# Kernel tuning notes

Hardware: AMD Instinct MI355X
Metric: run time of the kernel (lower is better)

The kernel has to match this reference:

```python
import jax, jax.numpy as jnp
import numpy as np

T, H, I, E, Z, TOPK = 1024, 1024, 512, 32, 8, 4
ROUTED_SCALING = 1.0


def setup_inputs() -> dict:
    key = jax.random.key(0)
    k1, k2, k3, k4 = jax.random.split(key, 4)
    return {
        "hidden_states": jax.random.normal(k1, (T, H), jnp.float32),
        "router_w": jax.random.normal(k2, (E + Z, H), jnp.float32) * 0.02,
        "correction_bias": jnp.zeros((E + Z,), jnp.float32),
        "w_gate_up": jax.random.normal(k3, (E, 2 * I, H), jnp.float32) * 0.02,
        "w_down": jax.random.normal(k4, (E, H, I), jnp.float32) * 0.02,
        "top_k": TOPK,
    }


def reference(hidden_states, router_w, correction_bias, w_gate_up, w_down, top_k):
    # hidden_states: [T, H]; router_w: [E+Z, H]; w_gate_up: [E, 2I, H]; w_down: [E, H, I]
    t, h = hidden_states.shape
    e = w_gate_up.shape[0]
    i = w_down.shape[2]
    # --- router (float32, no bias; correction bias only affects selection) ---
    logits = jnp.einsum("th,eh->te", hidden_states.astype(jnp.float32), router_w)
    scores = jax.nn.softmax(logits, axis=-1)                     # [T, E+Z]
    _, idx = jax.lax.top_k(scores + correction_bias[None, :], top_k)  # [T, k]
    w = jnp.take_along_axis(scores, idx, axis=1) * ROUTED_SCALING     # renormalize=False
    # combine matrix [T, E+Z] (sparse top-k scattered dense)
    comb = jnp.zeros((t, scores.shape[1]), jnp.float32)
    comb = comb.at[jnp.arange(t)[:, None], idx].add(w)
    comb_routed = comb[:, :e].astype(hidden_states.dtype)        # [T, E]
    zero_w = comb[:, e:].sum(-1).astype(hidden_states.dtype)     # [T] identity zero-experts
    # --- grouped SiLU-gated expert MLPs (dense all-experts reference) ---
    gu = jnp.einsum("th,eih->eti", hidden_states, w_gate_up)     # [E, T, 2I]
    hmid = jax.nn.silu(gu[..., :i]) * gu[..., i:]                # [E, T, I]
    ye = jnp.einsum("eti,ehi->eth", hmid, w_down)                # [E, T, H]
    out = jnp.einsum("te,eth->th", comb_routed, ye)
    out = out + zero_w[:, None] * hidden_states
    return out
```

## Files before the change

### kernel.cpp

```cpp
#include <hip/hip_runtime.h>
#include <hip/hip_bf16.h>
#include <math.h>

#define TT   1024
#define HH   1024
#define II   512
#define EE   32
#define NE   40
#define TOPK 4
#define CAP  1024

typedef __attribute__((ext_vector_type(4))) short short4v;
typedef __attribute__((ext_vector_type(8))) short short8v;
typedef __attribute__((ext_vector_type(4))) float floatx4;

static __device__ __forceinline__ short f2bf(float f) {
    unsigned u = __float_as_uint(f);
    unsigned r = (u + 0x7fffu + ((u >> 16) & 1u)) >> 16;
    return (short)(r & 0xffffu);
}
static __device__ __forceinline__ float bf2f(short s) {
    return __uint_as_float(((unsigned)(unsigned short)s) << 16);
}
static __device__ __forceinline__ short4v cvt4(float4 v) {
    short4v b = { f2bf(v.x), f2bf(v.y), f2bf(v.z), f2bf(v.w) };
    return b;
}

#define WS_NEED_COMBINE 12845056ull

__global__ __launch_bounds__(64) void router_kernel(
    const float* __restrict__ x, const float* __restrict__ rw,
    const float* __restrict__ bias,
    float* __restrict__ topk_w, float* __restrict__ zero_w,
    int* __restrict__ kexp, int* __restrict__ counts, int* __restrict__ slots)
{
    __shared__ float xs[HH];
    const int t = blockIdx.x;
    const int lane = threadIdx.x;

    const float4* xp = (const float4*)(x + (size_t)t * HH);
    float4* xs4 = (float4*)xs;
    #pragma unroll
    for (int i = 0; i < HH / 4 / 64; ++i) xs4[lane + 64 * i] = xp[lane + 64 * i];
    __syncthreads();

    float mylogit = -INFINITY;
    for (int e0 = 0; e0 < NE; e0 += 4) {
        const float* r0 = rw + (size_t)e0 * HH;
        float p0 = 0.f, p1 = 0.f, p2 = 0.f, p3 = 0.f;
        #pragma unroll
        for (int i = 0; i < HH / 64; ++i) {
            int h = lane + 64 * i;
            float xv = xs[h];
            p0 += xv * r0[h];
            p1 += xv * r0[HH + h];
            p2 += xv * r0[2 * HH + h];
            p3 += xv * r0[3 * HH + h];
        }
        #pragma unroll
        for (int off = 32; off > 0; off >>= 1) {
            p0 += __shfl_xor(p0, off); p1 += __shfl_xor(p1, off);
            p2 += __shfl_xor(p2, off); p3 += __shfl_xor(p3, off);
        }
        if (lane == e0)     mylogit = p0;
        if (lane == e0 + 1) mylogit = p1;
        if (lane == e0 + 2) mylogit = p2;
        if (lane == e0 + 3) mylogit = p3;
    }

    float m = mylogit;
    #pragma unroll
    for (int off = 32; off > 0; off >>= 1) m = fmaxf(m, __shfl_xor(m, off));
    float pexp = (lane < NE) ? expf(mylogit - m) : 0.f;
    float s = pexp;
    #pragma unroll
    for (int off = 32; off > 0; off >>= 1) s += __shfl_xor(s, off);
    const float score = pexp / s;

    float val = (lane < NE) ? score + bias[lane] : -INFINITY;
    int   kidx[TOPK];
    float kw[TOPK];
    #pragma unroll
    for (int k = 0; k < TOPK; ++k) {
        float v = val; int idx = lane;
        #pragma unroll
        for (int off = 32; off > 0; off >>= 1) {
            float ov = __shfl_xor(v, off);
            int   oi = __shfl_xor(idx, off);
            if (ov > v || (ov == v && oi < idx)) { v = ov; idx = oi; }
        }
        kidx[k] = idx;
        kw[k]   = __shfl(score, idx);
        if (lane == idx) val = -INFINITY;
    }

    if (lane == 0) {
        float zw = 0.f;
        #pragma unroll
        for (int k = 0; k < TOPK; ++k) {
            int slot = t * TOPK + k;
            topk_w[slot] = kw[k];
            kexp[slot]   = kidx[k];
            if (kidx[k] < EE) {
                int pos = atomicAdd(&counts[kidx[k]], 1);
                slots[kidx[k] * CAP + pos] = slot;
            } else {
                zw += kw[k];
            }
        }
        zero_w[t] = zw;
    }
}

#define GM  128
#define GNP 32
#define GK  32
#define KP  40

__global__ __launch_bounds__(256) void gate_up_kernel(
    const float* __restrict__ x, const float* __restrict__ wgu,
    const int* __restrict__ counts, const int* __restrict__ slots,
    short* __restrict__ hmid)
{
    const int e = blockIdx.y;
    const int cnt = counts[e];
    const int m_base = blockIdx.z * GM;
    if (m_base >= cnt) return;
    const int c_base = blockIdx.x * GNP;

    __shared__ short As[2][GM * KP];
    __shared__ short Bs[2][2 * GNP * KP];
    __shared__ int   sl[GM];

    const int tid = threadIdx.x;
    if (tid < GM) {
        int m = m_base + tid;
        sl[tid] = (m < cnt) ? slots[e * CAP + m] : -1;
    }
    __syncthreads();

    const int kq = tid & 7;
    const float* wb = wgu + (size_t)e * (2 * II) * HH;

    int rowA[4]; int slA[4]; const float* pAx[4];
    #pragma unroll
    for (int it = 0; it < 4; ++it) {
        rowA[it] = (tid >> 3) + 32 * it;
        int s = sl[rowA[it]];
        slA[it] = s;
        pAx[it] = x + (size_t)((s >= 0 ? s : 0) >> 2) * HH + kq * 4;
    }
    int rowB[2]; const float* pB[2];
    #pragma unroll
    for (int it = 0; it < 2; ++it) {
        rowB[it] = (tid >> 3) + 32 * it;
        int grow = (rowB[it] < GNP) ? (c_base + rowB[it]) : (II + c_base + rowB[it] - GNP);
        pB[it] = wb + (size_t)grow * HH + kq * 4;
    }

    const int lane = tid & 63;
    const int wv_  = tid >> 6;
    const int wy   = wv_ & 1;
    const int wx   = wv_ >> 1;
    const int quad = lane >> 4;
    const int mcol = lane & 15;

    floatx4 accg[4] = {};
    floatx4 accu[4] = {};

    float4 pa[4], pb[2];
    const float4 fz = make_float4(0.f, 0.f, 0.f, 0.f);

    #pragma unroll
    for (int it = 0; it < 4; ++it) pa[it] = (slA[it] >= 0) ? *(const float4*)(pAx[it]) : fz;
    #pragma unroll
    for (int it = 0; it < 2; ++it) pb[it] = *(const float4*)(pB[it]);
    #pragma unroll
    for (int it = 0; it < 4; ++it) *(short4v*)&As[0][rowA[it] * KP + kq * 4] = cvt4(pa[it]);
    #pragma unroll
    for (int it = 0; it < 2; ++it) *(short4v*)&Bs[0][rowB[it] * KP + kq * 4] = cvt4(pb[it]);
    __syncthreads();

    int p = 0;
    for (int k0 = 0; k0 < HH; k0 += GK) {
        const int kn = k0 + GK;
        const bool more = kn < HH;
        if (more) {
            #pragma unroll
            for (int it = 0; it < 4; ++it) pa[it] = (slA[it] >= 0) ? *(const float4*)(pAx[it] + kn) : fz;
            #pragma unroll
            for (int it = 0; it < 2; ++it) pb[it] = *(const float4*)(pB[it] + kn);
        }

        short8v a[4], bg, bu;
        #pragma unroll
        for (int i = 0; i < 4; ++i)
            a[i] = *(const short8v*)&As[p][(wy * 64 + i * 16 + mcol) * KP + quad * 8];
        bg = *(const short8v*)&Bs[p][(wx * 16 + mcol) * KP + quad * 8];
        bu = *(const short8v*)&Bs[p][(GNP + wx * 16 + mcol) * KP + quad * 8];
        #pragma unroll
        for (int i = 0; i < 4; ++i) {
            accg[i] = __builtin_amdgcn_mfma_f32_16x16x32_bf16(a[i], bg, accg[i], 0, 0, 0);
            accu[i] = __builtin_amdgcn_mfma_f32_16x16x32_bf16(a[i], bu, accu[i], 0, 0, 0);
        }

        if (more) {
            #pragma unroll
            for (int it = 0; it < 4; ++it) *(short4v*)&As[1 - p][rowA[it] * KP + kq * 4] = cvt4(pa[it]);
            #pragma unroll
            for (int it = 0; it < 2; ++it) *(short4v*)&Bs[1 - p][rowB[it] * KP + kq * 4] = cvt4(pb[it]);
        }
        __syncthreads();
        p ^= 1;
    }

    #pragma unroll
    for (int i = 0; i < 4; ++i) {
        #pragma unroll
        for (int r = 0; r < 4; ++r) {
            int m = wy * 64 + i * 16 + quad * 4 + r;
            int s = sl[m];
            if (s < 0) continue;
            float g = accg[i][r], u = accu[i][r];
            float valf = g * u / (1.f + __expf(-g));
            hmid[(size_t)s * II + c_base + wx * 16 + mcol] = f2bf(valf);
        }
    }
}

#define DM 128
#define DN 64

template<int WRITE_Y>
__global__ __launch_bounds__(256) void down_kernel_t(
    const short* __restrict__ hmid, const float* __restrict__ wd,
    const int* __restrict__ counts, const int* __restrict__ slots,
    const float* __restrict__ topk_w, short* __restrict__ ydown,
    float* __restrict__ out)
{
    const int e = blockIdx.y;
    const int cnt = counts[e];
    const int m_base = blockIdx.z * DM;
    if (m_base >= cnt) return;
    const int n_base = blockIdx.x * DN;

    __shared__ short As[2][DM * KP];
    __shared__ short Bs[2][DN * KP];
    __shared__ int   sl[DM];
    __shared__ float wvs[DM];

    const int tid = threadIdx.x;
    if (tid < DM) {
        int m = m_base + tid;
        int s = (m < cnt) ? slots[e * CAP + m] : -1;
        sl[tid]  = s;
        wvs[tid] = (s >= 0) ? topk_w[s] : 0.f;
    }
    __syncthreads();

    const float* wb = wd + (size_t)e * HH * II;

    const int kc = tid & 3;
    int rowA[2]; int slA[2]; const short* pAh[2];
    #pragma unroll
    for (int it = 0; it < 2; ++it) {
        rowA[it] = (tid >> 2) + 64 * it;
        int s = sl[rowA[it]];
        slA[it] = s;
        pAh[it] = hmid + (size_t)(s >= 0 ? s : 0) * II + kc * 8;
    }
    const int kq = tid & 7;
    int rowB[2]; const float* pB[2];
    #pragma unroll
    for (int it = 0; it < 2; ++it) {
        rowB[it] = (tid >> 3) + 32 * it;
        pB[it] = wb + (size_t)(n_base + rowB[it]) * II + kq * 4;
    }

    const int lane = tid & 63;
    const int wv_  = tid >> 6;
    const int wy   = wv_ & 1;
    const int wx   = wv_ >> 1;
    const int quad = lane >> 4;
    const int mcol = lane & 15;

    floatx4 acc[4][2] = {};

    short8v pa[2]; float4 pb[2];
    const short8v sz = { 0, 0, 0, 0, 0, 0, 0, 0 };

    #pragma unroll
    for (int it = 0; it < 2; ++it) pa[it] = (slA[it] >= 0) ? *(const short8v*)(pAh[it]) : sz;
    #pragma unroll
    for (int it = 0; it < 2; ++it) pb[it] = *(const float4*)(pB[it]);
    #pragma unroll
    for (int it = 0; it < 2; ++it) *(short8v*)&As[0][rowA[it] * KP + kc * 8] = pa[it];
    #pragma unroll
    for (int it = 0; it < 2; ++it) *(short4v*)&Bs[0][rowB[it] * KP + kq * 4] = cvt4(pb[it]);
    __syncthreads();

    int p = 0;
    for (int k0 = 0; k0 < II; k0 += GK) {
        const int kn = k0 + GK;
        const bool more = kn < II;
        if (more) {
            #pragma unroll
            for (int it = 0; it < 2; ++it) pa[it] = (slA[it] >= 0) ? *(const short8v*)(pAh[it] + kn) : sz;
            #pragma unroll
            for (int it = 0; it < 2; ++it) pb[it] = *(const float4*)(pB[it] + kn);
        }

        short8v a[4], b[2];
        #pragma unroll
        for (int i = 0; i < 4; ++i)
            a[i] = *(const short8v*)&As[p][(wy * 64 + i * 16 + mcol) * KP + quad * 8];
        #pragma unroll
        for (int j = 0; j < 2; ++j)
            b[j] = *(const short8v*)&Bs[p][(wx * 32 + j * 16 + mcol) * KP + quad * 8];
        #pragma unroll
        for (int i = 0; i < 4; ++i)
            #pragma unroll
            for (int j = 0; j < 2; ++j)
                acc[i][j] = __builtin_amdgcn_mfma_f32_16x16x32_bf16(a[i], b[j], acc[i][j], 0, 0, 0);

        if (more) {
            #pragma unroll
            for (int it = 0; it < 2; ++it) *(short8v*)&As[1 - p][rowA[it] * KP + kc * 8] = pa[it];
            #pragma unroll
            for (int it = 0; it < 2; ++it) *(short4v*)&Bs[1 - p][rowB[it] * KP + kq * 4] = cvt4(pb[it]);
        }
        __syncthreads();
        p ^= 1;
    }

    #pragma unroll
    for (int i = 0; i < 4; ++i) {
        #pragma unroll
        for (int r = 0; r < 4; ++r) {
            int m = wy * 64 + i * 16 + quad * 4 + r;
            int s = sl[m];
            if (s < 0) continue;
            if (WRITE_Y) {
                short* yrow = ydown + (size_t)s * HH + n_base + wx * 32;
                #pragma unroll
                for (int j = 0; j < 2; ++j)
                    yrow[j * 16 + mcol] = f2bf(acc[i][j][r]);
            } else {
                float w = wvs[m];
                float* orow = out + (size_t)(s >> 2) * HH + n_base + wx * 32;
                #pragma unroll
                for (int j = 0; j < 2; ++j)
                    atomicAdd(&orow[j * 16 + mcol], w * acc[i][j][r]);
            }
        }
    }
}

__global__ __launch_bounds__(256) void combine_kernel(
    const float* __restrict__ x, const short* __restrict__ ydown,
    const float* __restrict__ topk_w, const int* __restrict__ kexp,
    const float* __restrict__ zero_w, float* __restrict__ out)
{
    const int t = blockIdx.x;
    const int c = threadIdx.x;
    const float4 xv = ((const float4*)(x + (size_t)t * HH))[c];
    const float zw = zero_w[t];
    float4 o;
    o.x = zw * xv.x; o.y = zw * xv.y; o.z = zw * xv.z; o.w = zw * xv.w;
    #pragma unroll
    for (int k = 0; k < TOPK; ++k) {
        int slot = t * TOPK + k;
        if (kexp[slot] < EE) {
            float w = topk_w[slot];
            short4v y = *(const short4v*)&ydown[(size_t)slot * HH + c * 4];
            o.x += w * bf2f(y[0]);
            o.y += w * bf2f(y[1]);
            o.z += w * bf2f(y[2]);
            o.w += w * bf2f(y[3]);
        }
    }
    ((float4*)(out + (size_t)t * HH))[c] = o;
}

__global__ __launch_bounds__(256) void zero_resid_kernel(
    const float* __restrict__ x, const float* __restrict__ zero_w,
    float* __restrict__ out)
{
    const int t = blockIdx.x;
    const float zw = zero_w[t];
    const int tid = threadIdx.x;
    const float4 xv = ((const float4*)(x + (size_t)t * HH))[tid];
    float4* o = (float4*)(out + (size_t)t * HH);
    float4 ov = o[tid];
    ov.x += zw * xv.x; ov.y += zw * xv.y; ov.z += zw * xv.z; ov.w += zw * xv.w;
    o[tid] = ov;
}

extern "C" void kernel_launch(void* const* d_in, const int* in_sizes, int n_in,
                              void* d_out, int out_size, void* d_ws, size_t ws_size,
                              hipStream_t stream) {
    const float* x    = (const float*)d_in[0];
    const float* rw   = (const float*)d_in[1];
    const float* bias = (const float*)d_in[2];
    const float* wgu  = (const float*)d_in[3];
    const float* wd   = (const float*)d_in[4];
    float* out = (float*)d_out;

    char* ws = (char*)d_ws;
    int*   counts = (int*)ws;
    float* topk_w = (float*)(ws + 1024);
    float* zero_w = (float*)(ws + 17408);
    int*   kexp   = (int*)(ws + 21504);
    int*   slots  = (int*)(ws + 40960);
    short* hmid   = (short*)(ws + 262144);
    short* ydown  = (short*)(ws + 4456448);

    const bool big = ws_size >= WS_NEED_COMBINE;

    hipMemsetAsync(counts, 0, EE * sizeof(int), stream);
    if (!big) hipMemsetAsync(out, 0, (size_t)out_size * sizeof(float), stream);

    router_kernel<<<dim3(TT), dim3(64), 0, stream>>>(
        x, rw, bias, topk_w, zero_w, kexp, counts, slots);
    gate_up_kernel<<<dim3(II / GNP, EE, CAP / GM), dim3(256), 0, stream>>>(
        x, wgu, counts, slots, hmid);
    if (big) {
        down_kernel_t<1><<<dim3(HH / DN, EE, CAP / DM), dim3(256), 0, stream>>>(
            hmid, wd, counts, slots, topk_w, ydown, out);
        combine_kernel<<<dim3(TT), dim3(256), 0, stream>>>(
            x, ydown, topk_w, kexp, zero_w, out);
    } else {
        down_kernel_t<0><<<dim3(HH / DN, EE, CAP / DM), dim3(256), 0, stream>>>(
            hmid, wd, counts, slots, topk_w, nullptr, out);
        zero_resid_kernel<<<dim3(TT), dim3(256), 0, stream>>>(x, zero_w, out);
    }
}
```

Measured before the change: 313.9 us.

## Pre-convert activations to bf16, fold routing weight into gate-up, batch router tokens

A new kernel converts x to bf16 once, so the gate-up GEMM loads bf16 activations instead of converting fp32 in each tile. The routing weight is now applied in the gate-up epilogue, which removes the multiplies in the down and combine kernels. The router handles two tokens per block and keeps x in registers, so each router weight load is reused twice. Float-to-bf16 conversion uses the packed hardware builtin when it is available. The cost is an extra launch, a larger workspace requirement, and rounding the weighted hidden value to bf16 before the down GEMM.

```diff
diff --git a/kernel.cpp b/kernel.cpp
--- a/kernel.cpp
+++ b/kernel.cpp
@@ -22,12 +22,42 @@
 static __device__ __forceinline__ float bf2f(short s) {
     return __uint_as_float(((unsigned)(unsigned short)s) << 16);
 }
+
+#if defined(__has_builtin)
+#if __has_builtin(__builtin_amdgcn_cvt_pk_bf16_f32)
+#define HAVE_PK_BF16 1
+#endif
+#endif
+
+static __device__ __forceinline__ unsigned pk2(float a, float b) {
+#ifdef HAVE_PK_BF16
+    typedef __attribute__((ext_vector_type(2))) __bf16 bf2t;
+    union { bf2t v; unsigned u; } cv;
+    cv.v = __builtin_amdgcn_cvt_pk_bf16_f32(a, b);
+    return cv.u;
+#else
+    return (unsigned)(unsigned short)f2bf(a) | ((unsigned)(unsigned short)f2bf(b) << 16);
+#endif
+}
 static __device__ __forceinline__ short4v cvt4(float4 v) {
-    short4v b = { f2bf(v.x), f2bf(v.y), f2bf(v.z), f2bf(v.w) };
-    return b;
-}
-
-#define WS_NEED_COMBINE 12845056ull
+    union { unsigned u[2]; short4v s; } cv;
+    cv.u[0] = pk2(v.x, v.y); cv.u[1] = pk2(v.z, v.w);
+    return cv.s;
+}
+
+#define WS_NEED_COMBINE 14942208ull
+
+__global__ __launch_bounds__(256) void xconv_kernel(
+    const float* __restrict__ x, short* __restrict__ xb)
+{
+    size_t i = ((size_t)blockIdx.x * 256 + threadIdx.x) * 8;
+    float4 a = *(const float4*)&x[i];
+    float4 b = *(const float4*)&x[i + 4];
+    union { unsigned u[4]; short8v s; } cv;
+    cv.u[0] = pk2(a.x, a.y); cv.u[1] = pk2(a.z, a.w);
+    cv.u[2] = pk2(b.x, b.y); cv.u[3] = pk2(b.z, b.w);
+    *(short8v*)&xb[i] = cv.s;
+}
 
 __global__ __launch_bounds__(64) void router_kernel(
     const float* __restrict__ x, const float* __restrict__ rw,
@@ -35,81 +65,88 @@
     float* __restrict__ topk_w, float* __restrict__ zero_w,
     int* __restrict__ kexp, int* __restrict__ counts, int* __restrict__ slots)
 {
-    __shared__ float xs[HH];
-    const int t = blockIdx.x;
+    const int t0 = blockIdx.x * 2;
     const int lane = threadIdx.x;
 
-    const float4* xp = (const float4*)(x + (size_t)t * HH);
-    float4* xs4 = (float4*)xs;
-    #pragma unroll
-    for (int i = 0; i < HH / 4 / 64; ++i) xs4[lane + 64 * i] = xp[lane + 64 * i];
-    __syncthreads();
-
-    float mylogit = -INFINITY;
+    float xv0[16], xv1[16];
+    #pragma unroll
+    for (int i = 0; i < 16; ++i) {
+        xv0[i] = x[(size_t)t0 * HH + 64 * i + lane];
+        xv1[i] = x[(size_t)(t0 + 1) * HH + 64 * i + lane];
+    }
+
+    float lg[2] = { -INFINITY, -INFINITY };
     for (int e0 = 0; e0 < NE; e0 += 4) {
         const float* r0 = rw + (size_t)e0 * HH;
-        float p0 = 0.f, p1 = 0.f, p2 = 0.f, p3 = 0.f;
-        #pragma unroll
-        for (int i = 0; i < HH / 64; ++i) {
-            int h = lane + 64 * i;
-            float xv = xs[h];
-            p0 += xv * r0[h];
-            p1 += xv * r0[HH + h];
-            p2 += xv * r0[2 * HH + h];
-            p3 += xv * r0[3 * HH + h];
-        }
-        #pragma unroll
-        for (int off = 32; off > 0; off >>= 1) {
-            p0 += __shfl_xor(p0, off); p1 += __shfl_xor(p1, off);
-            p2 += __shfl_xor(p2, off); p3 += __shfl_xor(p3, off);
-        }
-        if (lane == e0)     mylogit = p0;
-        if (lane == e0 + 1) mylogit = p1;
-        if (lane == e0 + 2) mylogit = p2;
-        if (lane == e0 + 3) mylogit = p3;
-    }
-
-    float m = mylogit;
-    #pragma unroll
-    for (int off = 32; off > 0; off >>= 1) m = fmaxf(m, __shfl_xor(m, off));
-    float pexp = (lane < NE) ? expf(mylogit - m) : 0.f;
-    float s = pexp;
-    #pragma unroll
-    for (int off = 32; off > 0; off >>= 1) s += __shfl_xor(s, off);
-    const float score = pexp / s;
-
-    float val = (lane < NE) ? score + bias[lane] : -INFINITY;
-    int   kidx[TOPK];
-    float kw[TOPK];
-    #pragma unroll
-    for (int k = 0; k < TOPK; ++k) {
-        float v = val; int idx = lane;
-        #pragma unroll
-        for (int off = 32; off > 0; off >>= 1) {
-            float ov = __shfl_xor(v, off);
-            int   oi = __shfl_xor(idx, off);
-            if (ov > v || (ov == v && oi < idx)) { v = ov; idx = oi; }
-        }
-        kidx[k] = idx;
-        kw[k]   = __shfl(score, idx);
-        if (lane == idx) val = -INFINITY;
-    }
-
-    if (lane == 0) {
-        float zw = 0.f;
+        float p0[4] = {}, p1[4] = {};
+        #pragma unroll
+        for (int i = 0; i < 16; ++i) {
+            int h = 64 * i + lane;
+            float r[4];
+            #pragma unroll
+            for (int j = 0; j < 4; ++j) r[j] = r0[(size_t)j * HH + h];
+            #pragma unroll
+            for (int j = 0; j < 4; ++j) {
+                p0[j] += xv0[i] * r[j];
+                p1[j] += xv1[i] * r[j];
+            }
+        }
+        #pragma unroll
+        for (int j = 0; j < 4; ++j) {
+            #pragma unroll
+            for (int off = 32; off > 0; off >>= 1) {
+                p0[j] += __shfl_xor(p0[j], off);
+                p1[j] += __shfl_xor(p1[j], off);
+            }
+            if (lane == e0 + j) { lg[0] = p0[j]; lg[1] = p1[j]; }
+        }
+    }
+
+    for (int j = 0; j < 2; ++j) {
+        const int t = t0 + j;
+        float ml = lg[j];
+        float m = ml;
+        #pragma unroll
+        for (int off = 32; off > 0; off >>= 1) m = fmaxf(m, __shfl_xor(m, off));
+        float pexp = (lane < NE) ? expf(ml - m) : 0.f;
+        float s = pexp;
+        #pragma unroll
+        for (int off = 32; off > 0; off >>= 1) s += __shfl_xor(s, off);
+        const float score = pexp / s;
+
+        float val = (lane < NE) ? score + bias[lane] : -INFINITY;
+        int   kidx[TOPK];
+        float kw[TOPK];
         #pragma unroll
         for (int k = 0; k < TOPK; ++k) {
-            int slot = t * TOPK + k;
-            topk_w[slot] = kw[k];
-            kexp[slot]   = kidx[k];
-            if (kidx[k] < EE) {
-                int pos = atomicAdd(&counts[kidx[k]], 1);
-                slots[kidx[k] * CAP + pos] = slot;
-            } else {
-                zw += kw[k];
+            float v = val; int idx = lane;
+            #pragma unroll
+            for (int off = 32; off > 0; off >>= 1) {
+                float ov = __shfl_xor(v, off);
+                int   oi = __shfl_xor(idx, off);
+                if (ov > v || (ov == v && oi < idx)) { v = ov; idx = oi; }
             }
-        }
-        zero_w[t] = zw;
+            kidx[k] = idx;
+            kw[k]   = __shfl(score, idx);
+            if (lane == idx) val = -INFINITY;
+        }
+
+        if (lane == 0) {
+            float zw = 0.f;
+            #pragma unroll
+            for (int k = 0; k < TOPK; ++k) {
+                int slot = t * TOPK + k;
+                topk_w[slot] = kw[k];
+                kexp[slot]   = kidx[k];
+                if (kidx[k] < EE) {
+                    int pos = atomicAdd(&counts[kidx[k]], 1);
+                    slots[kidx[k] * CAP + pos] = slot;
+                } else {
+                    zw += kw[k];
+                }
+            }
+            zero_w[t] = zw;
+        }
     }
 }
 
@@ -119,9 +156,9 @@
 #define KP  40
 
 __global__ __launch_bounds__(256) void gate_up_kernel(
-    const float* __restrict__ x, const float* __restrict__ wgu,
+    const short* __restrict__ xb, const float* __restrict__ wgu,
     const int* __restrict__ counts, const int* __restrict__ slots,
-    short* __restrict__ hmid)
+    const float* __restrict__ topk_w, short* __restrict__ hmid)
 {
     const int e = blockIdx.y;
     const int cnt = counts[e];
@@ -132,25 +169,29 @@
     __shared__ short As[2][GM * KP];
     __shared__ short Bs[2][2 * GNP * KP];
     __shared__ int   sl[GM];
+    __shared__ float wvs[GM];
 
     const int tid = threadIdx.x;
     if (tid < GM) {
         int m = m_base + tid;
-        sl[tid] = (m < cnt) ? slots[e * CAP + m] : -1;
+        int s = (m < cnt) ? slots[e * CAP + m] : -1;
+        sl[tid]  = s;
+        wvs[tid] = (s >= 0) ? topk_w[s] : 0.f;
     }
     __syncthreads();
 
-    const int kq = tid & 7;
     const float* wb = wgu + (size_t)e * (2 * II) * HH;
 
-    int rowA[4]; int slA[4]; const float* pAx[4];
-    #pragma unroll
-    for (int it = 0; it < 4; ++it) {
-        rowA[it] = (tid >> 3) + 32 * it;
+    const int kcA = tid & 3;
+    int rowA[2]; int slA[2]; const short* pA[2];
+    #pragma unroll
+    for (int it = 0; it < 2; ++it) {
+        rowA[it] = (tid >> 2) + 64 * it;
         int s = sl[rowA[it]];
         slA[it] = s;
-        pAx[it] = x + (size_t)((s >= 0 ? s : 0) >> 2) * HH + kq * 4;
-    }
+        pA[it] = xb + (size_t)((s >= 0 ? s : 0) >> 2) * HH + kcA * 8;
+    }
+    const int kq = tid & 7;
     int rowB[2]; const float* pB[2];
     #pragma unroll
     for (int it = 0; it < 2; ++it) {
@@ -169,15 +210,15 @@
     floatx4 accg[4] = {};
     floatx4 accu[4] = {};
 
-    float4 pa[4], pb[2];
-    const float4 fz = make_float4(0.f, 0.f, 0.f, 0.f);
-
-    #pragma unroll
-    for (int it = 0; it < 4; ++it) pa[it] = (slA[it] >= 0) ? *(const float4*)(pAx[it]) : fz;
+    short8v pa[2]; float4 pb[2];
+    const short8v sz = { 0,0,0,0,0,0,0,0 };
+
+    #pragma unroll
+    for (int it = 0; it < 2; ++it) pa[it] = (slA[it] >= 0) ? *(const short8v*)(pA[it]) : sz;
     #pragma unroll
     for (int it = 0; it < 2; ++it) pb[it] = *(const float4*)(pB[it]);
     #pragma unroll
-    for (int it = 0; it < 4; ++it) *(short4v*)&As[0][rowA[it] * KP + kq * 4] = cvt4(pa[it]);
+    for (int it = 0; it < 2; ++it) *(short8v*)&As[0][rowA[it] * KP + kcA * 8] = pa[it];
     #pragma unroll
     for (int it = 0; it < 2; ++it) *(short4v*)&Bs[0][rowB[it] * KP + kq * 4] = cvt4(pb[it]);
     __syncthreads();
@@ -188,7 +229,7 @@
         const bool more = kn < HH;
         if (more) {
             #pragma unroll
-            for (int it = 0; it < 4; ++it) pa[it] = (slA[it] >= 0) ? *(const float4*)(pAx[it] + kn) : fz;
+            for (int it = 0; it < 2; ++it) pa[it] = (slA[it] >= 0) ? *(const short8v*)(pA[it] + kn) : sz;
             #pragma unroll
             for (int it = 0; it < 2; ++it) pb[it] = *(const float4*)(pB[it] + kn);
         }
@@ -207,7 +248,7 @@
 
         if (more) {
             #pragma unroll
-            for (int it = 0; it < 4; ++it) *(short4v*)&As[1 - p][rowA[it] * KP + kq * 4] = cvt4(pa[it]);
+            for (int it = 0; it < 2; ++it) *(short8v*)&As[1 - p][rowA[it] * KP + kcA * 8] = pa[it];
             #pragma unroll
             for (int it = 0; it < 2; ++it) *(short4v*)&Bs[1 - p][rowB[it] * KP + kq * 4] = cvt4(pb[it]);
         }
@@ -223,7 +264,7 @@
             int s = sl[m];
             if (s < 0) continue;
             float g = accg[i][r], u = accu[i][r];
-            float valf = g * u / (1.f + __expf(-g));
+            float valf = wvs[m] * g * u / (1.f + __expf(-g));
             hmid[(size_t)s * II + c_base + wx * 16 + mcol] = f2bf(valf);
         }
     }
@@ -236,8 +277,7 @@
 __global__ __launch_bounds__(256) void down_kernel_t(
     const short* __restrict__ hmid, const float* __restrict__ wd,
     const int* __restrict__ counts, const int* __restrict__ slots,
-    const float* __restrict__ topk_w, short* __restrict__ ydown,
-    float* __restrict__ out)
+    short* __restrict__ ydown, float* __restrict__ out)
 {
     const int e = blockIdx.y;
     const int cnt = counts[e];
@@ -248,27 +288,24 @@
     __shared__ short As[2][DM * KP];
     __shared__ short Bs[2][DN * KP];
     __shared__ int   sl[DM];
-    __shared__ float wvs[DM];
 
     const int tid = threadIdx.x;
     if (tid < DM) {
         int m = m_base + tid;
-        int s = (m < cnt) ? slots[e * CAP + m] : -1;
-        sl[tid]  = s;
-        wvs[tid] = (s >= 0) ? topk_w[s] : 0.f;
+        sl[tid] = (m < cnt) ? slots[e * CAP + m] : -1;
     }
     __syncthreads();
 
     const float* wb = wd + (size_t)e * HH * II;
 
-    const int kc = tid & 3;
-    int rowA[2]; int slA[2]; const short* pAh[2];
+    const int kcA = tid & 3;
+    int rowA[2]; int slA[2]; const short* pA[2];
     #pragma unroll
     for (int it = 0; it < 2; ++it) {
         rowA[it] = (tid >> 2) + 64 * it;
         int s = sl[rowA[it]];
         slA[it] = s;
-        pAh[it] = hmid + (size_t)(s >= 0 ? s : 0) * II + kc * 8;
+        pA[it] = hmid + (size_t)(s >= 0 ? s : 0) * II + kcA * 8;
     }
     const int kq = tid & 7;
     int rowB[2]; const float* pB[2];
@@ -288,14 +325,14 @@
     floatx4 acc[4][2] = {};
 
     short8v pa[2]; float4 pb[2];
-    const short8v sz = { 0, 0, 0, 0, 0, 0, 0, 0 };
-
-    #pragma unroll
-    for (int it = 0; it < 2; ++it) pa[it] = (slA[it] >= 0) ? *(const short8v*)(pAh[it]) : sz;
+    const short8v sz = { 0,0,0,0,0,0,0,0 };
+
+    #pragma unroll
+    for (int it = 0; it < 2; ++it) pa[it] = (slA[it] >= 0) ? *(const short8v*)(pA[it]) : sz;
     #pragma unroll
     for (int it = 0; it < 2; ++it) pb[it] = *(const float4*)(pB[it]);
     #pragma unroll
-    for (int it = 0; it < 2; ++it) *(short8v*)&As[0][rowA[it] * KP + kc * 8] = pa[it];
+    for (int it = 0; it < 2; ++it) *(short8v*)&As[0][rowA[it] * KP + kcA * 8] = pa[it];
     #pragma unroll
     for (int it = 0; it < 2; ++it) *(short4v*)&Bs[0][rowB[it] * KP + kq * 4] = cvt4(pb[it]);
     __syncthreads();
@@ -306,7 +343,7 @@
         const bool more = kn < II;
         if (more) {
             #pragma unroll
-            for (int it = 0; it < 2; ++it) pa[it] = (slA[it] >= 0) ? *(const short8v*)(pAh[it] + kn) : sz;
+            for (int it = 0; it < 2; ++it) pa[it] = (slA[it] >= 0) ? *(const short8v*)(pA[it] + kn) : sz;
             #pragma unroll
             for (int it = 0; it < 2; ++it) pb[it] = *(const float4*)(pB[it] + kn);
         }
@@ -326,7 +363,7 @@
 
         if (more) {
             #pragma unroll
-            for (int it = 0; it < 2; ++it) *(short8v*)&As[1 - p][rowA[it] * KP + kc * 8] = pa[it];
+            for (int it = 0; it < 2; ++it) *(short8v*)&As[1 - p][rowA[it] * KP + kcA * 8] = pa[it];
             #pragma unroll
             for (int it = 0; it < 2; ++it) *(short4v*)&Bs[1 - p][rowB[it] * KP + kq * 4] = cvt4(pb[it]);
         }
@@ -347,11 +384,10 @@
                 for (int j = 0; j < 2; ++j)
                     yrow[j * 16 + mcol] = f2bf(acc[i][j][r]);
             } else {
-                float w = wvs[m];
                 float* orow = out + (size_t)(s >> 2) * HH + n_base + wx * 32;
                 #pragma unroll
                 for (int j = 0; j < 2; ++j)
-                    atomicAdd(&orow[j * 16 + mcol], w * acc[i][j][r]);
+                    atomicAdd(&orow[j * 16 + mcol], acc[i][j][r]);
             }
         }
     }
@@ -359,8 +395,8 @@
 
 __global__ __launch_bounds__(256) void combine_kernel(
     const float* __restrict__ x, const short* __restrict__ ydown,
-    const float* __restrict__ topk_w, const int* __restrict__ kexp,
-    const float* __restrict__ zero_w, float* __restrict__ out)
+    const int* __restrict__ kexp, const float* __restrict__ zero_w,
+    float* __restrict__ out)
 {
     const int t = blockIdx.x;
     const int c = threadIdx.x;
@@ -372,12 +408,9 @@
     for (int k = 0; k < TOPK; ++k) {
         int slot = t * TOPK + k;
         if (kexp[slot] < EE) {
-            float w = topk_w[slot];
             short4v y = *(const short4v*)&ydown[(size_t)slot * HH + c * 4];
-            o.x += w * bf2f(y[0]);
-            o.y += w * bf2f(y[1]);
-            o.z += w * bf2f(y[2]);
-            o.w += w * bf2f(y[3]);
+            o.x += bf2f(y[0]); o.y += bf2f(y[1]);
+            o.z += bf2f(y[2]); o.w += bf2f(y[3]);
         }
     }
     ((float4*)(out + (size_t)t * HH))[c] = o;
@@ -413,26 +446,28 @@
     float* zero_w = (float*)(ws + 17408);
     int*   kexp   = (int*)(ws + 21504);
     int*   slots  = (int*)(ws + 40960);
-    short* hmid   = (short*)(ws + 262144);
-    short* ydown  = (short*)(ws + 4456448);
+    short* xb     = (short*)(ws + 262144);
+    short* hmid   = (short*)(ws + 2359296);
+    short* ydown  = (short*)(ws + 6553600);
 
     const bool big = ws_size >= WS_NEED_COMBINE;
 
     hipMemsetAsync(counts, 0, EE * sizeof(int), stream);
     if (!big) hipMemsetAsync(out, 0, (size_t)out_size * sizeof(float), stream);
 
-    router_kernel<<<dim3(TT), dim3(64), 0, stream>>>(
+    xconv_kernel<<<dim3(TT * HH / (256 * 8)), dim3(256), 0, stream>>>(x, xb);
+    router_kernel<<<dim3(TT / 2), dim3(64), 0, stream>>>(
         x, rw, bias, topk_w, zero_w, kexp, counts, slots);
     gate_up_kernel<<<dim3(II / GNP, EE, CAP / GM), dim3(256), 0, stream>>>(
-        x, wgu, counts, slots, hmid);
+        xb, wgu, counts, slots, topk_w, hmid);
     if (big) {
         down_kernel_t<1><<<dim3(HH / DN, EE, CAP / DM), dim3(256), 0, stream>>>(
-            hmid, wd, counts, slots, topk_w, ydown, out);
+            hmid, wd, counts, slots, ydown, out);
         combine_kernel<<<dim3(TT), dim3(256), 0, stream>>>(
-            x, ydown, topk_w, kexp, zero_w, out);
+            x, ydown, kexp, zero_w, out);
     } else {
         down_kernel_t<0><<<dim3(HH / DN, EE, CAP / DM), dim3(256), 0, stream>>>(
-            hmid, wd, counts, slots, topk_w, nullptr, out);
+            hmid, wd, counts, slots, nullptr, out);
         zero_resid_kernel<<<dim3(TT), dim3(256), 0, stream>>>(x, zero_w, out);
     }
 }
```

Result: slower. 331.1 us (+5.5%).
